# Optimization experiments

Hardware: AMD Instinct MI355X
Metric: run time of the kernel (lower is better)

## Reference

```python
import jax, jax.numpy as jnp
import numpy as np

N, E, ND, ED, H1, H2 = 50000, 800000, 128, 16, 256, 32
NEG_SLOPE = 0.2


def setup_inputs() -> dict:
    key = jax.random.key(0)
    ks = jax.random.split(key, 12)
    s = lambda k, shape: jax.random.normal(k, shape, jnp.float32) * 0.05
    return dict(
        x=jax.random.normal(ks[0], (N, ND), jnp.float32),
        edge_index=jax.random.randint(ks[1], (2, E), 0, N),
        edge_attr=jax.random.normal(ks[2], (E, ED), jnp.float32),
        Wl1=s(ks[3], (H1, ND)), bl1=jnp.zeros((H1,), jnp.float32),
        Wr1=s(ks[4], (H1, ND)), br1=jnp.zeros((H1,), jnp.float32),
        We1=s(ks[5], (H1, ED)), att1=s(ks[6], (H1,)), bias1=jnp.zeros((H1,), jnp.float32),
        Wl2=s(ks[7], (H2, H1)), bl2=jnp.zeros((H2,), jnp.float32),
        Wr2=s(ks[8], (H2, H1)), br2=jnp.zeros((H2,), jnp.float32),
        We2=s(ks[9], (H2, ED)), att2=s(ks[10], (H2,)), bias2=jnp.zeros((H2,), jnp.float32),
    )


def _gatv2_layer(x, src, dst, ea, Wl, bl, Wr, br, We, att, bias, n):
    # heads=1, concat=True  (PyG GATv2Conv defaults)
    xl = x @ Wl.T + bl                      # [n, C]  source transform
    xr = x @ Wr.T + br                      # [n, C]  target transform
    # per-edge message: x_j + x_i + lin_edge(edge_attr), then LeakyReLU
    m = jax.nn.leaky_relu(xl[src] + xr[dst] + ea @ We.T, NEG_SLOPE)  # [Etot, C]
    logit = m @ att                         # [Etot]
    # segment softmax over destination nodes (numerically stable)
    lmax = jax.ops.segment_max(logit, dst, num_segments=n)
    lmax = jnp.where(jnp.isfinite(lmax), lmax, 0.0)
    a = jnp.exp(logit - lmax[dst])
    denom = jax.ops.segment_sum(a, dst, num_segments=n)
    a = a / denom[dst]                      # self-loops guarantee denom > 0
    # scatter-add of alpha-weighted source features, plus output bias
    return jax.ops.segment_sum(xl[src] * a[:, None], dst, num_segments=n) + bias


def reference(x, edge_index, edge_attr,
              Wl1, bl1, Wr1, br1, We1, att1, bias1,
              Wl2, bl2, Wr2, br2, We2, att2, bias2):
    n = x.shape[0]
    src, dst = edge_index[0], edge_index[1]
    # add_self_loops=True with fill_value='mean': loop attr = mean incoming edge_attr
    deg = jax.ops.segment_sum(jnp.ones_like(dst, jnp.float32), dst, num_segments=n)
    loop_attr = jax.ops.segment_sum(edge_attr, dst, num_segments=n) / jnp.maximum(deg, 1.0)[:, None]
    loop = jnp.arange(n)
    src_f = jnp.concatenate([src, loop])
    dst_f = jnp.concatenate([dst, loop])
    ea = jnp.concatenate([edge_attr, loop_attr], axis=0)
    h = _gatv2_layer(x, src_f, dst_f, ea, Wl1, bl1, Wr1, br1, We1, att1, bias1, n)
    h = _gatv2_layer(h, src_f, dst_f, ea, Wl2, bl2, Wr2, br2, We2, att2, bias2, n)
    return h.mean(axis=0)  # [out_dim]
```

## Files before the change

### kernel.cpp

```cpp
#include <hip/hip_runtime.h>
#include <math.h>

#define N_NODES 50000
#define N_EDGES 800000
#define ND 128
#define ED 16
#define H1 256
#define H2 32

typedef short bf16x8 __attribute__((ext_vector_type(8)));
typedef float f32x4 __attribute__((ext_vector_type(4)));

__device__ __forceinline__ float dot2h(uint a, uint b, float c) {
    asm("v_dot2_f32_f16 %0, %1, %2, %0" : "+v"(c) : "v"(a), "v"(b));
    return c;
}
__device__ __forceinline__ float fmamix_lo(uint a, float b, float c) {
    float d;
    asm("v_fma_mix_f32 %0, %1, %2, %3 op_sel_hi:[1,0,0]" : "=v"(d) : "v"(a), "v"(b), "v"(c));
    return d;
}
__device__ __forceinline__ float fmamix_hi(uint a, float b, float c) {
    float d;
    asm("v_fma_mix_f32 %0, %1, %2, %3 op_sel:[1,0,0] op_sel_hi:[1,0,0]" : "=v"(d) : "v"(a), "v"(b), "v"(c));
    return d;
}
__device__ __forceinline__ ushort f2bf(float f) {
    uint u = __float_as_uint(f);
    return (ushort)((u + 0x7fff + ((u >> 16) & 1)) >> 16);
}

__global__ void k_deg(const int* __restrict__ ei, int* __restrict__ counts, int E) {
    int e = blockIdx.x * blockDim.x + threadIdx.x;
    if (e < E) atomicAdd(&counts[ei[E + e]], 1);
}

__global__ void k_scan1(const int* __restrict__ counts, int* __restrict__ partial, int n, int chunk) {
    __shared__ int sh[256];
    int beg = blockIdx.x * chunk, end = min(beg + chunk, n);
    int sum = 0;
    for (int i = beg + threadIdx.x; i < end; i += 256) sum += counts[i] + 1;
    sh[threadIdx.x] = sum;
    __syncthreads();
    for (int off = 128; off; off >>= 1) {
        if (threadIdx.x < off) sh[threadIdx.x] += sh[threadIdx.x + off];
        __syncthreads();
    }
    if (threadIdx.x == 0) partial[blockIdx.x] = sh[0];
}
__global__ void k_scan2(int* __restrict__ partial) {
    __shared__ int sh[256];
    int v = partial[threadIdx.x];
    sh[threadIdx.x] = v;
    __syncthreads();
    for (int off = 1; off < 256; off <<= 1) {
        int t = (threadIdx.x >= off) ? sh[threadIdx.x - off] : 0;
        __syncthreads();
        sh[threadIdx.x] += t;
        __syncthreads();
    }
    partial[threadIdx.x] = sh[threadIdx.x] - v;
}
__global__ void k_scan3(const int* __restrict__ counts, const int* __restrict__ partial,
                        int* __restrict__ rowptr, int n, int chunk) {
    __shared__ int sh[256];
    int beg = blockIdx.x * chunk, end = min(beg + chunk, n);
    int run = partial[blockIdx.x];
    for (int base = beg; base < end; base += 256) {
        int i = base + threadIdx.x;
        int v = (i < end) ? counts[i] + 1 : 0;
        sh[threadIdx.x] = v;
        __syncthreads();
        for (int off = 1; off < 256; off <<= 1) {
            int t = (threadIdx.x >= off) ? sh[threadIdx.x - off] : 0;
            __syncthreads();
            sh[threadIdx.x] += t;
            __syncthreads();
        }
        if (i < end) rowptr[i + 1] = run + sh[threadIdx.x];
        __syncthreads();
        run += sh[255];
        __syncthreads();
    }
    if (blockIdx.x == 0 && threadIdx.x == 0) rowptr[0] = 0;
}

__global__ void k_fill_csr(const int* __restrict__ ei, const float* __restrict__ ea,
                           const int* __restrict__ rowptr, int* __restrict__ fill,
                           int* __restrict__ csr_src, _Float16* __restrict__ ea_h, int E, int n) {
    int idx = blockIdx.x * blockDim.x + threadIdx.x;
    if (idx < E) {
        int dst = ei[E + idx];
        int slot = rowptr[dst] + atomicAdd(&fill[dst], 1);
        csr_src[slot] = ei[idx];
        const float* srow = ea + (size_t)idx * ED;
        _Float16* drow = ea_h + (size_t)slot * ED;
        #pragma unroll
        for (int q = 0; q < 4; ++q) {
            float4 f = ((const float4*)srow)[q];
            drow[q * 4 + 0] = (_Float16)f.x;
            drow[q * 4 + 1] = (_Float16)f.y;
            drow[q * 4 + 2] = (_Float16)f.z;
            drow[q * 4 + 3] = (_Float16)f.w;
        }
    } else if (idx < E + n) {
        int i = idx - E;
        csr_src[rowptr[i + 1] - 1] = i;
    }
}

__global__ void k_loop_mean(_Float16* __restrict__ ea_h, const int* __restrict__ rowptr, int n) {
    int idx = blockIdx.x * blockDim.x + threadIdx.x;
    if (idx >= n * ED) return;
    int node = idx >> 4, d = idx & 15;
    int beg = rowptr[node], last = rowptr[node + 1] - 1;
    float s = 0.f;
    for (int j = beg; j < last; ++j) s += (float)ea_h[(size_t)j * ED + d];
    int cnt = last - beg;
    ea_h[(size_t)last * ED + d] = (_Float16)(s / (float)(cnt > 0 ? cnt : 1));
}

__global__ void k_pack_half(const float* __restrict__ src, _Float16* __restrict__ dst, int total) {
    int i = blockIdx.x * blockDim.x + threadIdx.x;
    if (i < total) dst[i] = (_Float16)src[i];
}
__global__ void k_pack_bf16x4(const float* __restrict__ src, ushort* __restrict__ dst, int total4) {
    int i = blockIdx.x * blockDim.x + threadIdx.x;
    if (i >= total4) return;
    float4 f = ((const float4*)src)[i];
    ushort4 o;
    o.x = f2bf(f.x); o.y = f2bf(f.y); o.z = f2bf(f.z); o.w = f2bf(f.w);
    ((ushort4*)dst)[i] = o;
}
__global__ void k_pack_wcat(const float* __restrict__ Wa, const float* __restrict__ Wb,
                            ushort* __restrict__ dst, int C, int K) {
    int i = blockIdx.x * blockDim.x + threadIdx.x;
    if (i >= 2 * C * K) return;
    int row = i / K, k = i - row * K;
    float v = (row < C) ? Wa[(size_t)row * K + k] : Wb[(size_t)(row - C) * K + k];
    dst[i] = f2bf(v);
}

template <int HALF_A>
__global__ __launch_bounds__(256) void k_gemm_mfma(const ushort* __restrict__ Xb,
                                                   const ushort* __restrict__ Wc,
                                                   const float* __restrict__ ba,
                                                   const float* __restrict__ bb,
                                                   void* __restrict__ Ya,
                                                   float* __restrict__ Yb,
                                                   int n, int K, int C) {
    int tid = threadIdx.x;
    int lane = tid & 63, wv = tid >> 6;
    int r = lane & 15, kg = lane >> 4;
    int row0 = blockIdx.x * 64 + wv * 16;
    int colblk = blockIdx.y * 64;
    int arow = row0 + r;
    if (arow >= n) arow = n - 1;
    const ushort* aptr = Xb + (size_t)arow * K + kg * 8;
    f32x4 acc[4] = {};
    for (int k0 = 0; k0 < K; k0 += 32) {
        bf16x8 av = *(const bf16x8*)(aptr + k0);
        #pragma unroll
        for (int t = 0; t < 4; ++t) {
            const ushort* bptr = Wc + (size_t)(colblk + t * 16 + r) * K + k0 + kg * 8;
            bf16x8 bv = *(const bf16x8*)bptr;
            acc[t] = __builtin_amdgcn_mfma_f32_16x16x32_bf16(av, bv, acc[t], 0, 0, 0);
        }
    }
    #pragma unroll
    for (int t = 0; t < 4; ++t) {
        int col = colblk + t * 16 + r;
        int rowb = row0 + kg * 4;
        #pragma unroll
        for (int q = 0; q < 4; ++q) {
            int row = rowb + q;
            if (row >= n) continue;
            float v = acc[t][q];
            if (col < C) {
                v += ba[col];
                if (HALF_A) ((_Float16*)Ya)[(size_t)row * C + col] = (_Float16)v;
                else        ((float*)Ya)[(size_t)row * C + col] = v;
            } else {
                Yb[(size_t)row * C + (col - C)] = v + bb[col - C];
            }
        }
    }
}

__global__ __launch_bounds__(256) void k_gat1(const _Float16* __restrict__ xlh,
                                              const float* __restrict__ xr,
                                              const _Float16* __restrict__ ea_h,
                                              const _Float16* __restrict__ We_h,
                                              const float* __restrict__ att,
                                              const float* __restrict__ bias,
                                              const int* __restrict__ rowptr,
                                              const int* __restrict__ csr_src,
                                              ushort* __restrict__ out_bf, int n) {
    const int lane = threadIdx.x & 63;
    int wave = (blockIdx.x * blockDim.x + threadIdx.x) >> 6;
    int nwaves = (gridDim.x * blockDim.x) >> 6;
    const uint* Wp = (const uint*)We_h;
    uint w0[8], w1[8], w2[8], w3[8];
    #pragma unroll
    for (int q = 0; q < 8; ++q) {
        w0[q] = Wp[(lane * 4 + 0) * 8 + q];
        w1[q] = Wp[(lane * 4 + 1) * 8 + q];
        w2[q] = Wp[(lane * 4 + 2) * 8 + q];
        w3[q] = Wp[(lane * 4 + 3) * 8 + q];
    }
    float4 attv = ((const float4*)att)[lane];
    float4 bv = ((const float4*)bias)[lane];
    float a06x = 0.6f * attv.x, a06y = 0.6f * attv.y, a06z = 0.6f * attv.z, a06w = 0.6f * attv.w;
    float a04x = 0.4f * attv.x, a04y = 0.4f * attv.y, a04z = 0.4f * attv.z, a04w = 0.4f * attv.w;
    const float fone = 1.0f;
    const uint laneoff = (uint)lane << 3;

    for (int node = wave; node < n; node += nwaves) {
        float4 xrv = *(const float4*)(xr + ((size_t)node << 8) + (lane << 2));
        int beg = rowptr[node], end = rowptr[node + 1];
        float denom = 0.f, ac0 = 0.f, ac1 = 0.f, ac2 = 0.f, ac3 = 0.f;
        int j = beg;
        for (; j + 1 < end; j += 2) {
            int sA = __builtin_amdgcn_readfirstlane(csr_src[j]);
            int sB = __builtin_amdgcn_readfirstlane(csr_src[j + 1]);
            const uint4* eP = (const uint4*)((const char*)ea_h + ((uint)j << 5));
            uint4 eA0 = eP[0], eA1 = eP[1], eB0 = eP[2], eB1 = eP[3];
            uint2 xA = *(const uint2*)((const char*)xlh + (((uint)sA << 9) + laneoff));
            uint2 xB = *(const uint2*)((const char*)xlh + (((uint)sB << 9) + laneoff));
            float weA0 = dot2h(w0[7], eA1.w, dot2h(w0[6], eA1.z, dot2h(w0[5], eA1.y, dot2h(w0[4], eA1.x,
                         dot2h(w0[3], eA0.w, dot2h(w0[2], eA0.z, dot2h(w0[1], eA0.y, dot2h(w0[0], eA0.x, 0.f))))))));
            float weA1 = dot2h(w1[7], eA1.w, dot2h(w1[6], eA1.z, dot2h(w1[5], eA1.y, dot2h(w1[4], eA1.x,
                         dot2h(w1[3], eA0.w, dot2h(w1[2], eA0.z, dot2h(w1[1], eA0.y, dot2h(w1[0], eA0.x, 0.f))))))));
            float weA2 = dot2h(w2[7], eA1.w, dot2h(w2[6], eA1.z, dot2h(w2[5], eA1.y, dot2h(w2[4], eA1.x,
                         dot2h(w2[3], eA0.w, dot2h(w2[2], eA0.z, dot2h(w2[1], eA0.y, dot2h(w2[0], eA0.x, 0.f))))))));
            float weA3 = dot2h(w3[7], eA1.w, dot2h(w3[6], eA1.z, dot2h(w3[5], eA1.y, dot2h(w3[4], eA1.x,
                         dot2h(w3[3], eA0.w, dot2h(w3[2], eA0.z, dot2h(w3[1], eA0.y, dot2h(w3[0], eA0.x, 0.f))))))));
            float weB0 = dot2h(w0[7], eB1.w, dot2h(w0[6], eB1.z, dot2h(w0[5], eB1.y, dot2h(w0[4], eB1.x,
                         dot2h(w0[3], eB0.w, dot2h(w0[2], eB0.z, dot2h(w0[1], eB0.y, dot2h(w0[0], eB0.x, 0.f))))))));
            float weB1 = dot2h(w1[7], eB1.w, dot2h(w1[6], eB1.z, dot2h(w1[5], eB1.y, dot2h(w1[4], eB1.x,
                         dot2h(w1[3], eB0.w, dot2h(w1[2], eB0.z, dot2h(w1[1], eB0.y, dot2h(w1[0], eB0.x, 0.f))))))));
            float weB2 = dot2h(w2[7], eB1.w, dot2h(w2[6], eB1.z, dot2h(w2[5], eB1.y, dot2h(w2[4], eB1.x,
                         dot2h(w2[3], eB0.w, dot2h(w2[2], eB0.z, dot2h(w2[1], eB0.y, dot2h(w2[0], eB0.x, 0.f))))))));
            float weB3 = dot2h(w3[7], eB1.w, dot2h(w3[6], eB1.z, dot2h(w3[5], eB1.y, dot2h(w3[4], eB1.x,
                         dot2h(w3[3], eB0.w, dot2h(w3[2], eB0.z, dot2h(w3[1], eB0.y, dot2h(w3[0], eB0.x, 0.f))))))));
            float zA0 = fmamix_lo(xA.x, fone, weA0 + xrv.x);
            float zA1 = fmamix_hi(xA.x, fone, weA1 + xrv.y);
            float zA2 = fmamix_lo(xA.y, fone, weA2 + xrv.z);
            float zA3 = fmamix_hi(xA.y, fone, weA3 + xrv.w);
            float zB0 = fmamix_lo(xB.x, fone, weB0 + xrv.x);
            float zB1 = fmamix_hi(xB.x, fone, weB1 + xrv.y);
            float zB2 = fmamix_lo(xB.y, fone, weB2 + xrv.z);
            float zB3 = fmamix_hi(xB.y, fone, weB3 + xrv.w);
            float pA = fmaf(a06x, zA0, fmaf(a04x, fabsf(zA0),
                       fmaf(a06y, zA1, fmaf(a04y, fabsf(zA1),
                       fmaf(a06z, zA2, fmaf(a04z, fabsf(zA2),
                       fmaf(a06w, zA3, a04w * fabsf(zA3))))))));
            float pB = fmaf(a06x, zB0, fmaf(a04x, fabsf(zB0),
                       fmaf(a06y, zB1, fmaf(a04y, fabsf(zB1),
                       fmaf(a06z, zB2, fmaf(a04z, fabsf(zB2),
                       fmaf(a06w, zB3, a04w * fabsf(zB3))))))));
            #pragma unroll
            for (int off = 32; off >= 1; off >>= 1) {
                pA += __shfl_xor(pA, off);
                pB += __shfl_xor(pB, off);
            }
            float peA = __expf(pA), peB = __expf(pB);
            denom += peA + peB;
            ac0 = fmamix_lo(xB.x, peB, fmamix_lo(xA.x, peA, ac0));
            ac1 = fmamix_hi(xB.x, peB, fmamix_hi(xA.x, peA, ac1));
            ac2 = fmamix_lo(xB.y, peB, fmamix_lo(xA.y, peA, ac2));
            ac3 = fmamix_hi(xB.y, peB, fmamix_hi(xA.y, peA, ac3));
        }
        if (j < end) {
            int sA = __builtin_amdgcn_readfirstlane(csr_src[j]);
            const uint4* eP = (const uint4*)((const char*)ea_h + ((uint)j << 5));
            uint4 eA0 = eP[0], eA1 = eP[1];
            uint2 xA = *(const uint2*)((const char*)xlh + (((uint)sA << 9) + laneoff));
            float weA0 = dot2h(w0[7], eA1.w, dot2h(w0[6], eA1.z, dot2h(w0[5], eA1.y, dot2h(w0[4], eA1.x,
                         dot2h(w0[3], eA0.w, dot2h(w0[2], eA0.z, dot2h(w0[1], eA0.y, dot2h(w0[0], eA0.x, 0.f))))))));
            float weA1 = dot2h(w1[7], eA1.w, dot2h(w1[6], eA1.z, dot2h(w1[5], eA1.y, dot2h(w1[4], eA1.x,
                         dot2h(w1[3], eA0.w, dot2h(w1[2], eA0.z, dot2h(w1[1], eA0.y, dot2h(w1[0], eA0.x, 0.f))))))));
            float weA2 = dot2h(w2[7], eA1.w, dot2h(w2[6], eA1.z, dot2h(w2[5], eA1.y, dot2h(w2[4], eA1.x,
                         dot2h(w2[3], eA0.w, dot2h(w2[2], eA0.z, dot2h(w2[1], eA0.y, dot2h(w2[0], eA0.x, 0.f))))))));
            float weA3 = dot2h(w3[7], eA1.w, dot2h(w3[6], eA1.z, dot2h(w3[5], eA1.y, dot2h(w3[4], eA1.x,
                         dot2h(w3[3], eA0.w, dot2h(w3[2], eA0.z, dot2h(w3[1], eA0.y, dot2h(w3[0], eA0.x, 0.f))))))));
            float zA0 = fmamix_lo(xA.x, fone, weA0 + xrv.x);
            float zA1 = fmamix_hi(xA.x, fone, weA1 + xrv.y);
            float zA2 = fmamix_lo(xA.y, fone, weA2 + xrv.z);
            float zA3 = fmamix_hi(xA.y, fone, weA3 + xrv.w);
            float pA = fmaf(a06x, zA0, fmaf(a04x, fabsf(zA0),
                       fmaf(a06y, zA1, fmaf(a04y, fabsf(zA1),
                       fmaf(a06z, zA2, fmaf(a04z, fabsf(zA2),
                       fmaf(a06w, zA3, a04w * fabsf(zA3))))))));
            #pragma unroll
            for (int off = 32; off >= 1; off >>= 1) pA += __shfl_xor(pA, off);
            float peA = __expf(pA);
            denom += peA;
            ac0 = fmamix_lo(xA.x, peA, ac0);
            ac1 = fmamix_hi(xA.x, peA, ac1);
            ac2 = fmamix_lo(xA.y, peA, ac2);
            ac3 = fmamix_hi(xA.y, peA, ac3);
        }
        float inv = 1.f / denom;
        ushort4 o;
        o.x = f2bf(fmaf(ac0, inv, bv.x));
        o.y = f2bf(fmaf(ac1, inv, bv.y));
        o.z = f2bf(fmaf(ac2, inv, bv.z));
        o.w = f2bf(fmaf(ac3, inv, bv.w));
        *(ushort4*)(out_bf + ((size_t)node << 8) + (lane << 2)) = o;
    }
}

__global__ __launch_bounds__(256) void k_gat2(const float* __restrict__ xl,
                                              const float* __restrict__ xr,
                                              const _Float16* __restrict__ ea_h,
                                              const _Float16* __restrict__ We_h,
                                              const float* __restrict__ att,
                                              const float* __restrict__ bias,
                                              const int* __restrict__ rowptr,
                                              const int* __restrict__ csr_src,
                                              float* __restrict__ out, int n) {
    int tid = threadIdx.x;
    int lane = tid & 63;
    int sub = lane >> 5, c = lane & 31;
    int wave = (blockIdx.x * blockDim.x + tid) >> 6;
    int nwaves = (gridDim.x * blockDim.x) >> 6;
    const uint* Wp = (const uint*)We_h;
    uint w0 = Wp[c * 8 + 0], w1 = Wp[c * 8 + 1], w2 = Wp[c * 8 + 2], w3 = Wp[c * 8 + 3];
    uint w4 = Wp[c * 8 + 4], w5 = Wp[c * 8 + 5], w6 = Wp[c * 8 + 6], w7 = Wp[c * 8 + 7];
    float attc = att[c];
    float a06 = 0.6f * attc, a04 = 0.4f * attc;
    float bc = bias[c];

    for (int node = wave; node < n; node += nwaves) {
        float xrc = xr[((size_t)node << 5) + c];
        int beg = rowptr[node], end = rowptr[node + 1];
        float denom = 0.f, acc = 0.f;
        for (int j = beg; j < end; j += 2) {
            int jj = j + sub;
            bool act = jj < end;
            int js = act ? jj : j;
            int s = csr_src[js];
            const uint4* eP = (const uint4*)((const char*)ea_h + ((uint)js << 5));
            uint4 e0 = eP[0], e1 = eP[1];
            float xlv = *(const float*)((const char*)xl + (((uint)s << 7) + (c << 2)));
            float we = dot2h(w7, e1.w, dot2h(w6, e1.z, dot2h(w5, e1.y, dot2h(w4, e1.x,
                       dot2h(w3, e0.w, dot2h(w2, e0.z, dot2h(w1, e0.y, dot2h(w0, e0.x, 0.f))))))));
            float z = xlv + xrc + we;
            float p = fmaf(a06, z, a04 * fabsf(z));
            #pragma unroll
            for (int off = 16; off >= 1; off >>= 1) p += __shfl_xor(p, off);
            float pe = act ? __expf(p) : 0.f;
            denom += pe;
            acc = fmaf(pe, xlv, acc);
        }
        acc += __shfl_xor(acc, 32);
        denom += __shfl_xor(denom, 32);
        if (sub == 0) out[((size_t)node << 5) + c] = acc / denom + bc;
    }
}

__global__ __launch_bounds__(256) void k_mean(const float* __restrict__ h2,
                                              float* __restrict__ out, int total, float invN) {
    __shared__ float red[H2];
    int tid = threadIdx.x;
    if (tid < H2) red[tid] = 0.f;
    __syncthreads();
    float part = 0.f;
    for (int idx = blockIdx.x * blockDim.x + tid; idx < total; idx += gridDim.x * blockDim.x)
        part += h2[idx];
    atomicAdd(&red[tid & 31], part);
    __syncthreads();
    if (tid < H2) atomicAdd(&out[tid], red[tid] * invN);
}

extern "C" void kernel_launch(void* const* d_in, const int* in_sizes, int n_in,
                              void* d_out, int out_size, void* d_ws, size_t ws_size,
                              hipStream_t stream) {
    const float* x   = (const float*)d_in[0];
    const int*   ei  = (const int*)d_in[1];
    const float* ea  = (const float*)d_in[2];
    const float* Wl1 = (const float*)d_in[3];
    const float* bl1 = (const float*)d_in[4];
    const float* Wr1 = (const float*)d_in[5];
    const float* br1 = (const float*)d_in[6];
    const float* We1 = (const float*)d_in[7];
    const float* at1 = (const float*)d_in[8];
    const float* bi1 = (const float*)d_in[9];
    const float* Wl2 = (const float*)d_in[10];
    const float* bl2 = (const float*)d_in[11];
    const float* Wr2 = (const float*)d_in[12];
    const float* br2 = (const float*)d_in[13];
    const float* We2 = (const float*)d_in[14];
    const float* at2 = (const float*)d_in[15];
    const float* bi2 = (const float*)d_in[16];
    float* out = (float*)d_out;

    const int N = N_NODES, E = N_EDGES, ET = N_EDGES + N_NODES;
    const int SCAN_CHUNK = (N + 255) / 256;

    size_t off = 0;
    auto carve = [&](size_t bytes) {
        void* p = (char*)d_ws + off;
        off += (bytes + 255) & ~(size_t)255;
        return p;
    };
    int*      counts  = (int*)carve((size_t)N * 4);
    int*      fill    = (int*)carve((size_t)N * 4);
    int*      rowptr  = (int*)carve((size_t)(N + 1) * 4);
    int*      partial = (int*)carve(256 * 4);
    int*      csr_src = (int*)carve((size_t)ET * 4);
    _Float16* ea_h    = (_Float16*)carve((size_t)ET * ED * 2);
    _Float16* We1_h   = (_Float16*)carve((size_t)H1 * ED * 2);
    _Float16* We2_h   = (_Float16*)carve((size_t)H2 * ED * 2);
    ushort*   x_bf    = (ushort*)carve((size_t)N * ND * 2);
    ushort*   wcat1   = (ushort*)carve((size_t)2 * H1 * ND * 2);
    ushort*   wcat2   = (ushort*)carve((size_t)2 * H2 * H1 * 2);
    _Float16* xl1h    = (_Float16*)carve((size_t)N * H1 * 2);
    float*    xr1     = (float*)carve((size_t)N * H1 * 4);
    ushort*   h1_bf   = (ushort*)carve((size_t)N * H1 * 2);
    float*    xl2     = (float*)carve((size_t)N * H2 * 4);
    float*    xr2     = (float*)carve((size_t)N * H2 * 4);
    float*    h2      = (float*)carve((size_t)N * H2 * 4);

    hipMemsetAsync(counts, 0, (size_t)N * 4, stream);
    hipMemsetAsync(fill, 0, (size_t)N * 4, stream);
    hipMemsetAsync(out, 0, (size_t)H2 * 4, stream);

    k_deg<<<(E + 255) / 256, 256, 0, stream>>>(ei, counts, E);
    k_scan1<<<256, 256, 0, stream>>>(counts, partial, N, SCAN_CHUNK);
    k_scan2<<<1, 256, 0, stream>>>(partial);
    k_scan3<<<256, 256, 0, stream>>>(counts, partial, rowptr, N, SCAN_CHUNK);
    k_fill_csr<<<(E + N + 255) / 256, 256, 0, stream>>>(ei, ea, rowptr, fill, csr_src, ea_h, E, N);
    k_loop_mean<<<(N * ED + 255) / 256, 256, 0, stream>>>(ea_h, rowptr, N);
    k_pack_half<<<(H1 * ED + 255) / 256, 256, 0, stream>>>(We1, We1_h, H1 * ED);
    k_pack_half<<<(H2 * ED + 255) / 256, 256, 0, stream>>>(We2, We2_h, H2 * ED);
    k_pack_bf16x4<<<(N * ND / 4 + 255) / 256, 256, 0, stream>>>(x, x_bf, N * ND / 4);
    k_pack_wcat<<<(2 * H1 * ND + 255) / 256, 256, 0, stream>>>(Wl1, Wr1, wcat1, H1, ND);
    k_pack_wcat<<<(2 * H2 * H1 + 255) / 256, 256, 0, stream>>>(Wl2, Wr2, wcat2, H2, H1);

    k_gemm_mfma<1><<<dim3((N + 63) / 64, (2 * H1) / 64), 256, 0, stream>>>(
        x_bf, wcat1, bl1, br1, (void*)xl1h, xr1, N, ND, H1);
    k_gat1<<<4096, 256, 0, stream>>>(xl1h, xr1, ea_h, We1_h, at1, bi1,
                                     rowptr, csr_src, h1_bf, N);

    k_gemm_mfma<0><<<dim3((N + 63) / 64, (2 * H2) / 64), 256, 0, stream>>>(
        h1_bf, wcat2, bl2, br2, (void*)xl2, xr2, N, H1, H2);
    k_gat2<<<12500, 256, 0, stream>>>(xl2, xr2, ea_h, We2_h, at2, bi2,
                                      rowptr, csr_src, h2, N);

    k_mean<<<128, 256, 0, stream>>>(h2, out, N * H2, 1.0f / (float)N);
}
```

Before: 501.0 us.

## Unroll GAT edge loops by four and coalesce self-loop mean reduction

k_gat1 now processes four edges per iteration instead of two, using a shared logit helper, so more independent gathers and shuffle reductions are in flight per wave. k_gat2 gets a four-edge main loop (two per half-wave) with no predication, and the old predicated loop is kept only as the tail. k_loop_mean switches from one thread per (node, dim) doing strided scalar half loads to one wave per node, where 8 lane groups each read 4-byte half2 chunks and the partial sums are combined with cross-lane shuffles. These changes target memory latency and uncoalesced access, at the cost of higher register pressure in the unrolled loops.

```diff
diff --git a/kernel.cpp b/kernel.cpp
--- a/kernel.cpp
+++ b/kernel.cpp
@@ -10,6 +10,7 @@
 
 typedef short bf16x8 __attribute__((ext_vector_type(8)));
 typedef float f32x4 __attribute__((ext_vector_type(4)));
+typedef _Float16 half2v __attribute__((ext_vector_type(2)));
 
 __device__ __forceinline__ float dot2h(uint a, uint b, float c) {
     asm("v_dot2_f32_f16 %0, %1, %2, %0" : "+v"(c) : "v"(a), "v"(b));
@@ -109,15 +110,35 @@
     }
 }
 
-__global__ void k_loop_mean(_Float16* __restrict__ ea_h, const int* __restrict__ rowptr, int n) {
-    int idx = blockIdx.x * blockDim.x + threadIdx.x;
-    if (idx >= n * ED) return;
-    int node = idx >> 4, d = idx & 15;
-    int beg = rowptr[node], last = rowptr[node + 1] - 1;
-    float s = 0.f;
-    for (int j = beg; j < last; ++j) s += (float)ea_h[(size_t)j * ED + d];
-    int cnt = last - beg;
-    ea_h[(size_t)last * ED + d] = (_Float16)(s / (float)(cnt > 0 ? cnt : 1));
+__global__ __launch_bounds__(256) void k_loop_mean(_Float16* __restrict__ ea_h,
+                                                   const int* __restrict__ rowptr, int n) {
+    int lane = threadIdx.x & 63;
+    int wave = (blockIdx.x * blockDim.x + threadIdx.x) >> 6;
+    int nwaves = (gridDim.x * blockDim.x) >> 6;
+    int g = lane >> 3, q = lane & 7;
+    for (int node = wave; node < n; node += nwaves) {
+        int beg = rowptr[node], last = rowptr[node + 1] - 1;
+        float sx = 0.f, sy = 0.f;
+        for (int r = beg + g; r < last; r += 8) {
+            uint v = *(const uint*)((const char*)ea_h + ((uint)r << 5) + (q << 2));
+            half2v h = __builtin_bit_cast(half2v, v);
+            sx += (float)h.x;
+            sy += (float)h.y;
+        }
+        #pragma unroll
+        for (int off = 8; off <= 32; off <<= 1) {
+            sx += __shfl_xor(sx, off);
+            sy += __shfl_xor(sy, off);
+        }
+        if (lane < 8) {
+            int cnt = last - beg;
+            float inv = 1.f / (float)(cnt > 0 ? cnt : 1);
+            half2v o;
+            o.x = (_Float16)(sx * inv);
+            o.y = (_Float16)(sy * inv);
+            *(uint*)((char*)ea_h + ((uint)last << 5) + (q << 2)) = __builtin_bit_cast(uint, o);
+        }
+    }
 }
 
 __global__ void k_pack_half(const float* __restrict__ src, _Float16* __restrict__ dst, int total) {
@@ -187,6 +208,31 @@
     }
 }
 
+__device__ __forceinline__ float logit1(const uint (&w)[4][8], uint4 e0, uint4 e1,
+                                        uint2 xv, float4 xrv, float4 a06, float4 a04) {
+    float we[4];
+    #pragma unroll
+    for (int r = 0; r < 4; ++r) {
+        float s = dot2h(w[r][0], e0.x, 0.f);
+        s = dot2h(w[r][1], e0.y, s);
+        s = dot2h(w[r][2], e0.z, s);
+        s = dot2h(w[r][3], e0.w, s);
+        s = dot2h(w[r][4], e1.x, s);
+        s = dot2h(w[r][5], e1.y, s);
+        s = dot2h(w[r][6], e1.z, s);
+        s = dot2h(w[r][7], e1.w, s);
+        we[r] = s;
+    }
+    float z0 = fmamix_lo(xv.x, 1.0f, we[0] + xrv.x);
+    float z1 = fmamix_hi(xv.x, 1.0f, we[1] + xrv.y);
+    float z2 = fmamix_lo(xv.y, 1.0f, we[2] + xrv.z);
+    float z3 = fmamix_hi(xv.y, 1.0f, we[3] + xrv.w);
+    return fmaf(a06.x, z0, fmaf(a04.x, fabsf(z0),
+           fmaf(a06.y, z1, fmaf(a04.y, fabsf(z1),
+           fmaf(a06.z, z2, fmaf(a04.z, fabsf(z2),
+           fmaf(a06.w, z3, a04.w * fabsf(z3))))))));
+}
+
 __global__ __launch_bounds__(256) void k_gat1(const _Float16* __restrict__ xlh,
                                               const float* __restrict__ xr,
                                               const _Float16* __restrict__ ea_h,
@@ -200,19 +246,16 @@
     int wave = (blockIdx.x * blockDim.x + threadIdx.x) >> 6;
     int nwaves = (gridDim.x * blockDim.x) >> 6;
     const uint* Wp = (const uint*)We_h;
-    uint w0[8], w1[8], w2[8], w3[8];
+    uint w[4][8];
     #pragma unroll
-    for (int q = 0; q < 8; ++q) {
-        w0[q] = Wp[(lane * 4 + 0) * 8 + q];
-        w1[q] = Wp[(lane * 4 + 1) * 8 + q];
-        w2[q] = Wp[(lane * 4 + 2) * 8 + q];
-        w3[q] = Wp[(lane * 4 + 3) * 8 + q];
-    }
+    for (int r = 0; r < 4; ++r)
+        #pragma unroll
+        for (int q = 0; q < 8; ++q) w[r][q] = Wp[(lane * 4 + r) * 8 + q];
     float4 attv = ((const float4*)att)[lane];
     float4 bv = ((const float4*)bias)[lane];
-    float a06x = 0.6f * attv.x, a06y = 0.6f * attv.y, a06z = 0.6f * attv.z, a06w = 0.6f * attv.w;
-    float a04x = 0.4f * attv.x, a04y = 0.4f * attv.y, a04z = 0.4f * attv.z, a04w = 0.4f * attv.w;
-    const float fone = 1.0f;
+    float4 a06, a04;
+    a06.x = 0.6f * attv.x; a06.y = 0.6f * attv.y; a06.z = 0.6f * attv.z; a06.w = 0.6f * attv.w;
+    a04.x = 0.4f * attv.x; a04.y = 0.4f * attv.y; a04.z = 0.4f * attv.z; a04.w = 0.4f * attv.w;
     const uint laneoff = (uint)lane << 3;
 
     for (int node = wave; node < n; node += nwaves) {
@@ -220,86 +263,53 @@
         int beg = rowptr[node], end = rowptr[node + 1];
         float denom = 0.f, ac0 = 0.f, ac1 = 0.f, ac2 = 0.f, ac3 = 0.f;
         int j = beg;
-        for (; j + 1 < end; j += 2) {
-            int sA = __builtin_amdgcn_readfirstlane(csr_src[j]);
-            int sB = __builtin_amdgcn_readfirstlane(csr_src[j + 1]);
+        for (; j + 3 < end; j += 4) {
+            int s0 = __builtin_amdgcn_readfirstlane(csr_src[j]);
+            int s1 = __builtin_amdgcn_readfirstlane(csr_src[j + 1]);
+            int s2 = __builtin_amdgcn_readfirstlane(csr_src[j + 2]);
+            int s3 = __builtin_amdgcn_readfirstlane(csr_src[j + 3]);
             const uint4* eP = (const uint4*)((const char*)ea_h + ((uint)j << 5));
-            uint4 eA0 = eP[0], eA1 = eP[1], eB0 = eP[2], eB1 = eP[3];
-            uint2 xA = *(const uint2*)((const char*)xlh + (((uint)sA << 9) + laneoff));
-            uint2 xB = *(const uint2*)((const char*)xlh + (((uint)sB << 9) + laneoff));
-            float weA0 = dot2h(w0[7], eA1.w, dot2h(w0[6], eA1.z, dot2h(w0[5], eA1.y, dot2h(w0[4], eA1.x,
-                         dot2h(w0[3], eA0.w, dot2h(w0[2], eA0.z, dot2h(w0[1], eA0.y, dot2h(w0[0], eA0.x, 0.f))))))));
-            float weA1 = dot2h(w1[7], eA1.w, dot2h(w1[6], eA1.z, dot2h(w1[5], eA1.y, dot2h(w1[4], eA1.x,
-                         dot2h(w1[3], eA0.w, dot2h(w1[2], eA0.z, dot2h(w1[1], eA0.y, dot2h(w1[0], eA0.x, 0.f))))))));
-            float weA2 = dot2h(w2[7], eA1.w, dot2h(w2[6], eA1.z, dot2h(w2[5], eA1.y, dot2h(w2[4], eA1.x,
-                         dot2h(w2[3], eA0.w, dot2h(w2[2], eA0.z, dot2h(w2[1], eA0.y, dot2h(w2[0], eA0.x, 0.f))))))));
-            float weA3 = dot2h(w3[7], eA1.w, dot2h(w3[6], eA1.z, dot2h(w3[5], eA1.y, dot2h(w3[4], eA1.x,
-                         dot2h(w3[3], eA0.w, dot2h(w3[2], eA0.z, dot2h(w3[1], eA0.y, dot2h(w3[0], eA0.x, 0.f))))))));
-            float weB0 = dot2h(w0[7], eB1.w, dot2h(w0[6], eB1.z, dot2h(w0[5], eB1.y, dot2h(w0[4], eB1.x,
-                         dot2h(w0[3], eB0.w, dot2h(w0[2], eB0.z, dot2h(w0[1], eB0.y, dot2h(w0[0], eB0.x, 0.f))))))));
-            float weB1 = dot2h(w1[7], eB1.w, dot2h(w1[6], eB1.z, dot2h(w1[5], eB1.y, dot2h(w1[4], eB1.x,
-                         dot2h(w1[3], eB0.w, dot2h(w1[2], eB0.z, dot2h(w1[1], eB0.y, dot2h(w1[0], eB0.x, 0.f))))))));
-            float weB2 = dot2h(w2[7], eB1.w, dot2h(w2[6], eB1.z, dot2h(w2[5], eB1.y, dot2h(w2[4], eB1.x,
-                         dot2h(w2[3], eB0.w, dot2h(w2[2], eB0.z, dot2h(w2[1], eB0.y, dot2h(w2[0], eB0.x, 0.f))))))));
-            float weB3 = dot2h(w3[7], eB1.w, dot2h(w3[6], eB1.z, dot2h(w3[5], eB1.y, dot2h(w3[4], eB1.x,
-                         dot2h(w3[3], eB0.w, dot2h(w3[2], eB0.z, dot2h(w3[1], eB0.y, dot2h(w3[0], eB0.x, 0.f))))))));
-            float zA0 = fmamix_lo(xA.x, fone, weA0 + xrv.x);
-            float zA1 = fmamix_hi(xA.x, fone, weA1 + xrv.y);
-            float zA2 = fmamix_lo(xA.y, fone, weA2 + xrv.z);
-            float zA3 = fmamix_hi(xA.y, fone, weA3 + xrv.w);
-            float zB0 = fmamix_lo(xB.x, fone, weB0 + xrv.x);
-            float zB1 = fmamix_hi(xB.x, fone, weB1 + xrv.y);
-            float zB2 = fmamix_lo(xB.y, fone, weB2 + xrv.z);
-            float zB3 = fmamix_hi(xB.y, fone, weB3 + xrv.w);
-            float pA = fmaf(a06x, zA0, fmaf(a04x, fabsf(zA0),
-                       fmaf(a06y, zA1, fmaf(a04y, fabsf(zA1),
-                       fmaf(a06z, zA2, fmaf(a04z, fabsf(zA2),
-                       fmaf(a06w, zA3, a04w * fabsf(zA3))))))));
-            float pB = fmaf(a06x, zB0, fmaf(a04x, fabsf(zB0),
-                       fmaf(a06y, zB1, fmaf(a04y, fabsf(zB1),
-                       fmaf(a06z, zB2, fmaf(a04z, fabsf(zB2),
-                       fmaf(a06w, zB3, a04w * fabsf(zB3))))))));
+            uint4 e00 = eP[0], e01 = eP[1], e10 = eP[2], e11 = eP[3];
+            uint4 e20 = eP[4], e21 = eP[5], e30 = eP[6], e31 = eP[7];
+            uint2 x0 = *(const uint2*)((const char*)xlh + (((uint)s0 << 9) + laneoff));
+            uint2 x1 = *(const uint2*)((const char*)xlh + (((uint)s1 << 9) + laneoff));
+            uint2 x2 = *(const uint2*)((const char*)xlh + (((uint)s2 << 9) + laneoff));
+            uint2 x3 = *(const uint2*)((const char*)xlh + (((uint)s3 << 9) + laneoff));
+            float p0 = logit1(w, e00, e01, x0, xrv, a06, a04);
+            float p1 = logit1(w, e10, e11, x1, xrv, a06, a04);
+            float p2 = logit1(w, e20, e21, x2, xrv, a06, a04);
+            float p3 = logit1(w, e30, e31, x3, xrv, a06, a04);
             #pragma unroll
             for (int off = 32; off >= 1; off >>= 1) {
-                pA += __shfl_xor(pA, off);
-                pB += __shfl_xor(pB, off);
+                p0 += __shfl_xor(p0, off);
+                p1 += __shfl_xor(p1, off);
+                p2 += __shfl_xor(p2, off);
+                p3 += __shfl_xor(p3, off);
             }
-            float peA = __expf(pA), peB = __expf(pB);
-            denom += peA + peB;
-            ac0 = fmamix_lo(xB.x, peB, fmamix_lo(xA.x, peA, ac0));
-            ac1 = fmamix_hi(xB.x, peB, fmamix_hi(xA.x, peA, ac1));
-            ac2 = fmamix_lo(xB.y, peB, fmamix_lo(xA.y, peA, ac2));
-            ac3 = fmamix_hi(xB.y, peB, fmamix_hi(xA.y, peA, ac3));
-        }
-        if (j < end) {
-            int sA = __builtin_amdgcn_readfirstlane(csr_src[j]);
+            float q0 = __expf(p0), q1 = __expf(p1);
+            float q2 = __expf(p2), q3 = __expf(p3);
+            denom += (q0 + q1) + (q2 + q3);
+            ac0 = fmamix_lo(x0.x, q0, ac0); ac1 = fmamix_hi(x0.x, q0, ac1);
+            ac2 = fmamix_lo(x0.y, q0, ac2); ac3 = fmamix_hi(x0.y, q0, ac3);
+            ac0 = fmamix_lo(x1.x, q1, ac0); ac1 = fmamix_hi(x1.x, q1, ac1);
+            ac2 = fmamix_lo(x1.y, q1, ac2); ac3 = fmamix_hi(x1.y, q1, ac3);
+            ac0 = fmamix_lo(x2.x, q2, ac0); ac1 = fmamix_hi(x2.x, q2, ac1);
+            ac2 = fmamix_lo(x2.y, q2, ac2); ac3 = fmamix_hi(x2.y, q2, ac3);
+            ac0 = fmamix_lo(x3.x, q3, ac0); ac1 = fmamix_hi(x3.x, q3, ac1);
+            ac2 = fmamix_lo(x3.y, q3, ac2); ac3 = fmamix_hi(x3.y, q3, ac3);
+        }
+        for (; j < end; ++j) {
+            int s0 = __builtin_amdgcn_readfirstlane(csr_src[j]);
             const uint4* eP = (const uint4*)((const char*)ea_h + ((uint)j << 5));
-            uint4 eA0 = eP[0], eA1 = eP[1];
-            uint2 xA = *(const uint2*)((const char*)xlh + (((uint)sA << 9) + laneoff));
-            float weA0 = dot2h(w0[7], eA1.w, dot2h(w0[6], eA1.z, dot2h(w0[5], eA1.y, dot2h(w0[4], eA1.x,
-                         dot2h(w0[3], eA0.w, dot2h(w0[2], eA0.z, dot2h(w0[1], eA0.y, dot2h(w0[0], eA0.x, 0.f))))))));
-            float weA1 = dot2h(w1[7], eA1.w, dot2h(w1[6], eA1.z, dot2h(w1[5], eA1.y, dot2h(w1[4], eA1.x,
-                         dot2h(w1[3], eA0.w, dot2h(w1[2], eA0.z, dot2h(w1[1], eA0.y, dot2h(w1[0], eA0.x, 0.f))))))));
-            float weA2 = dot2h(w2[7], eA1.w, dot2h(w2[6], eA1.z, dot2h(w2[5], eA1.y, dot2h(w2[4], eA1.x,
-                         dot2h(w2[3], eA0.w, dot2h(w2[2], eA0.z, dot2h(w2[1], eA0.y, dot2h(w2[0], eA0.x, 0.f))))))));
-            float weA3 = dot2h(w3[7], eA1.w, dot2h(w3[6], eA1.z, dot2h(w3[5], eA1.y, dot2h(w3[4], eA1.x,
-                         dot2h(w3[3], eA0.w, dot2h(w3[2], eA0.z, dot2h(w3[1], eA0.y, dot2h(w3[0], eA0.x, 0.f))))))));
-            float zA0 = fmamix_lo(xA.x, fone, weA0 + xrv.x);
-            float zA1 = fmamix_hi(xA.x, fone, weA1 + xrv.y);
-            float zA2 = fmamix_lo(xA.y, fone, weA2 + xrv.z);
-            float zA3 = fmamix_hi(xA.y, fone, weA3 + xrv.w);
-            float pA = fmaf(a06x, zA0, fmaf(a04x, fabsf(zA0),
-                       fmaf(a06y, zA1, fmaf(a04y, fabsf(zA1),
-                       fmaf(a06z, zA2, fmaf(a04z, fabsf(zA2),
-                       fmaf(a06w, zA3, a04w * fabsf(zA3))))))));
+            uint4 e00 = eP[0], e01 = eP[1];
+            uint2 x0 = *(const uint2*)((const char*)xlh + (((uint)s0 << 9) + laneoff));
+            float p0 = logit1(w, e00, e01, x0, xrv, a06, a04);
             #pragma unroll
-            for (int off = 32; off >= 1; off >>= 1) pA += __shfl_xor(pA, off);
-            float peA = __expf(pA);
-            denom += peA;
-            ac0 = fmamix_lo(xA.x, peA, ac0);
-            ac1 = fmamix_hi(xA.x, peA, ac1);
-            ac2 = fmamix_lo(xA.y, peA, ac2);
-            ac3 = fmamix_hi(xA.y, peA, ac3);
+            for (int off = 32; off >= 1; off >>= 1) p0 += __shfl_xor(p0, off);
+            float q0 = __expf(p0);
+            denom += q0;
+            ac0 = fmamix_lo(x0.x, q0, ac0); ac1 = fmamix_hi(x0.x, q0, ac1);
+            ac2 = fmamix_lo(x0.y, q0, ac2); ac3 = fmamix_hi(x0.y, q0, ac3);
         }
         float inv = 1.f / denom;
         ushort4 o;
@@ -336,7 +346,34 @@
         float xrc = xr[((size_t)node << 5) + c];
         int beg = rowptr[node], end = rowptr[node + 1];
         float denom = 0.f, acc = 0.f;
-        for (int j = beg; j < end; j += 2) {
+        int j = beg;
+        for (; j + 3 < end; j += 4) {
+            int jA = j + sub, jB = j + 2 + sub;
+            int sA = csr_src[jA], sB = csr_src[jB];
+            const uint4* ePA = (const uint4*)((const char*)ea_h + ((uint)jA << 5));
+            const uint4* ePB = (const uint4*)((const char*)ea_h + ((uint)jB << 5));
+            uint4 a0 = ePA[0], a1 = ePA[1];
+            uint4 b0 = ePB[0], b1 = ePB[1];
+            float xlA = *(const float*)((const char*)xl + (((uint)sA << 7) + (c << 2)));
+            float xlB = *(const float*)((const char*)xl + (((uint)sB << 7) + (c << 2)));
+            float weA = dot2h(w7, a1.w, dot2h(w6, a1.z, dot2h(w5, a1.y, dot2h(w4, a1.x,
+                        dot2h(w3, a0.w, dot2h(w2, a0.z, dot2h(w1, a0.y, dot2h(w0, a0.x, 0.f))))))));
+            float weB = dot2h(w7, b1.w, dot2h(w6, b1.z, dot2h(w5, b1.y, dot2h(w4, b1.x,
+                        dot2h(w3, b0.w, dot2h(w2, b0.z, dot2h(w1, b0.y, dot2h(w0, b0.x, 0.f))))))));
+            float zA = xlA + xrc + weA;
+            float zB = xlB + xrc + weB;
+            float pA = fmaf(a06, zA, a04 * fabsf(zA));
+            float pB = fmaf(a06, zB, a04 * fabsf(zB));
+            #pragma unroll
+            for (int off = 16; off >= 1; off >>= 1) {
+                pA += __shfl_xor(pA, off);
+                pB += __shfl_xor(pB, off);
+            }
+            float qA = __expf(pA), qB = __expf(pB);
+            denom += qA + qB;
+            acc = fmaf(qA, xlA, fmaf(qB, xlB, acc));
+        }
+        for (; j < end; j += 2) {
             int jj = j + sub;
             bool act = jj < end;
             int js = act ? jj : j;
@@ -432,7 +469,7 @@
     k_scan2<<<1, 256, 0, stream>>>(partial);
     k_scan3<<<256, 256, 0, stream>>>(counts, partial, rowptr, N, SCAN_CHUNK);
     k_fill_csr<<<(E + N + 255) / 256, 256, 0, stream>>>(ei, ea, rowptr, fill, csr_src, ea_h, E, N);
-    k_loop_mean<<<(N * ED + 255) / 256, 256, 0, stream>>>(ea_h, rowptr, N);
+    k_loop_mean<<<1024, 256, 0, stream>>>(ea_h, rowptr, N);
     k_pack_half<<<(H1 * ED + 255) / 256, 256, 0, stream>>>(We1, We1_h, H1 * ED);
     k_pack_half<<<(H2 * ED + 255) / 256, 256, 0, stream>>>(We2, We2_h, H2 * ED);
     k_pack_bf16x4<<<(N * ND / 4 + 255) / 256, 256, 0, stream>>>(x, x_bf, N * ND / 4);
```

Result: faster. 478.3 us (-4.5%).
